# Performance work log

Measured on AMD Instinct MI355X. Metric: run time of the kernel, lower is better.

## Reference

```python
import jax, jax.numpy as jnp
import numpy as np

B, N, D, H = 8, 1024, 768, 12
HD = D // H
SCALE = HD ** -0.5

def setup_inputs() -> dict:
    key = jax.random.key(0)
    k1, k2, k3, k4 = jax.random.split(key, 4)
    x = jax.random.normal(k1, (B, N, D), dtype=jnp.float32)
    weight = jax.random.uniform(k2, (B, N), dtype=jnp.float32)
    W_qkv = jax.random.normal(k3, (D, 3 * D), dtype=jnp.float32) * (D ** -0.5)
    W_msa = jax.random.normal(k4, (D, D), dtype=jnp.float32) * (D ** -0.5)
    b_msa = jnp.zeros((D,), dtype=jnp.float32)
    return {"x": x, "weight": weight, "W_qkv": W_qkv, "W_msa": W_msa, "b_msa": b_msa}

def reference(x, weight, W_qkv, W_msa, b_msa):
    # QKV projection (no bias), then elementwise per-token gate
    qkv = jnp.einsum('bnd,de->bne', x, W_qkv)          # [B,N,3D]
    qkv = weight[:, :, None] * qkv
    qkv = qkv.reshape(B, N, 3, H, HD).transpose(2, 0, 3, 1, 4)  # [3,B,H,N,hd]
    q, k, v = qkv[0], qkv[1], qkv[2]
    A = jnp.einsum('bhnd,bhmd->bhnm', q, k) * SCALE    # [B,H,N,N]
    A = jax.nn.softmax(A, axis=-1)
    out = jnp.einsum('bhnm,bhmd->bhnd', A, v)          # [B,H,N,hd]
    out = out.transpose(0, 2, 1, 3).reshape(B, N, D)
    return jnp.einsum('bnd,de->bne', out, W_msa) + b_msa
```

## Files before the change

kernel.cpp:

```cpp
#include <hip/hip_runtime.h>
#include <hip/hip_bf16.h>


typedef __attribute__((ext_vector_type(8))) short bf8;
typedef __attribute__((ext_vector_type(4))) float f4;

#define QSCALE 0.1803368801111204f

static __device__ __forceinline__ short bf16_of(float f) {
    union { float f; unsigned u; } a; a.f = f;
    unsigned r = a.u + 0x7FFFu + ((a.u >> 16) & 1u);
    return (short)(r >> 16);
}

static __device__ __forceinline__ unsigned bfpk(float lo, float hi) {
    float2 t; t.x = lo; t.y = hi;
    __hip_bfloat162 b = __float22bfloat162_rn(t);
    union { __hip_bfloat162 b; unsigned u; } c; c.b = b;
    return c.u;
}

static __device__ __forceinline__ void async16(const short* g, short* l) {
    __builtin_amdgcn_global_load_lds(
        (const __attribute__((address_space(1))) void*)g,
        (__attribute__((address_space(3))) void*)l, 16, 0, 0);
}

__global__ __launch_bounds__(256) void k_cvt(const float* __restrict__ src,
                                             const float* __restrict__ gate,
                                             short* __restrict__ dst, int n8) {
    int i = blockIdx.x * 256 + threadIdx.x;
    if (i >= n8) return;
    const float g = gate[i / 96];
    const f4* sp = (const f4*)src;
    f4 a = sp[2 * i], b = sp[2 * i + 1];
    union { bf8 v; short h[8]; } o;
    o.h[0] = bf16_of(a[0] * g); o.h[1] = bf16_of(a[1] * g);
    o.h[2] = bf16_of(a[2] * g); o.h[3] = bf16_of(a[3] * g);
    o.h[4] = bf16_of(b[0] * g); o.h[5] = bf16_of(b[1] * g);
    o.h[6] = bf16_of(b[2] * g); o.h[7] = bf16_of(b[3] * g);
    ((bf8*)dst)[i] = o.v;
}

__global__ __launch_bounds__(256) void k_transpose(const float* __restrict__ w,
                                                   short* __restrict__ wt,
                                                   int K, int E) {
    __shared__ short t[64][65];
    const int k0 = blockIdx.y * 64, e0 = blockIdx.x * 64;
    const int tid = threadIdx.x;
#pragma unroll
    for (int p = 0; p < 16; ++p) {
        int idx = p * 256 + tid;
        int r = idx >> 6, c = idx & 63;
        t[r][c] = bf16_of(w[(k0 + r) * E + e0 + c]);
    }
    __syncthreads();
#pragma unroll
    for (int p = 0; p < 16; ++p) {
        int idx = p * 256 + tid;
        int r = idx >> 6, c = idx & 63;
        wt[(e0 + r) * K + k0 + c] = t[c][r];
    }
}

static __device__ __forceinline__ void gemm128(const short* __restrict__ gA,
                                               const short* __restrict__ gB,
                                               short* smem,
                                               f4 acc[4][4]) {
    const int tid = threadIdx.x, lane = tid & 63;
    const int l16 = lane & 15, quad = lane >> 4, rx = l16 & 7;
    const int wm = (tid >> 6) & 1, wn = tid >> 7;

    auto stage = [&](short* S, int k0) {
#pragma unroll
        for (int c = 0; c < 4; ++c) {
            int p = c * 256 + tid;
            int row = p >> 3, slot = p & 7;
            int gc = slot ^ (row & 7);
            async16(gA + row * 768 + k0 + gc * 8, S + p * 8);
            async16(gB + row * 768 + k0 + gc * 8, S + 8192 + p * 8);
        }
    };

    stage(smem, 0);
    for (int it = 0; it < 12; ++it) {
        __builtin_amdgcn_s_waitcnt(0);
        __syncthreads();
        short* Sc = smem + (it & 1) * 16384;
        if (it + 1 < 12) stage(smem + ((it + 1) & 1) * 16384, (it + 1) * 64);
        const short* As = Sc;
        const short* Bs = Sc + 8192;
#pragma unroll
        for (int ks = 0; ks < 2; ++ks) {
            bf8 af[4], bfr[4];
#pragma unroll
            for (int mt = 0; mt < 4; ++mt)
                af[mt] = *(const bf8*)(As + (wm * 64 + mt * 16 + l16) * 64 +
                                       (((ks * 4 + quad) ^ rx) * 8));
#pragma unroll
            for (int nt = 0; nt < 4; ++nt)
                bfr[nt] = *(const bf8*)(Bs + (wn * 64 + nt * 16 + l16) * 64 +
                                        (((ks * 4 + quad) ^ rx) * 8));
#pragma unroll
            for (int mt = 0; mt < 4; ++mt)
#pragma unroll
                for (int nt = 0; nt < 4; ++nt)
                    acc[mt][nt] = __builtin_amdgcn_mfma_f32_16x16x32_bf16(
                        af[mt], bfr[nt], acc[mt][nt], 0, 0, 0);
        }
    }
    __syncthreads();
}

__global__ __launch_bounds__(512, 2) void k_gemm_qkv(
        const short* __restrict__ xb, const short* __restrict__ wtq,
        short* __restrict__ qb, short* __restrict__ kb, short* __restrict__ vt) {
    __shared__ short lds[65536];
    const int tid = threadIdx.x, lane = tid & 63;
    const int l16 = lane & 15, quad = lane >> 4, rx = l16 & 7;
    const int wv = tid >> 6, wm = wv >> 2, wn = wv & 3;

    const int wg = blockIdx.x;
    const int swz = (wg & 7) * 36 + (wg >> 3);
    const int mI = swz / 9, nI = swz - mI * 9;
    const int m0 = mI * 256, n0 = nI * 256;

    const short* gA = xb + m0 * 768;
    const short* gB = wtq + n0 * 768;

    auto stageHalf = [&](int buf, int isB, int half, const short* gsrc, int k0) {
        short* dst = lds + buf * 32768 + isB * 16384 + half * 8192;
        const short* src = gsrc + half * 98304 + k0;
#pragma unroll
        for (int j = 0; j < 2; ++j) {
            int p = j * 512 + tid;
            int row = p >> 3;
            int gc = (p & 7) ^ (row & 7);
            async16(src + row * 768 + gc * 8, dst + p * 8);
        }
    };

    f4 z = {0.f, 0.f, 0.f, 0.f};
    f4 acc[8][4];
#pragma unroll
    for (int mt = 0; mt < 8; ++mt)
#pragma unroll
        for (int nt = 0; nt < 4; ++nt) acc[mt][nt] = z;

    stageHalf(0, 0, 0, gA, 0); stageHalf(0, 0, 1, gA, 0);
    stageHalf(0, 1, 0, gB, 0); stageHalf(0, 1, 1, gB, 0);
    stageHalf(1, 1, 0, gB, 64); stageHalf(1, 1, 1, gB, 64);
    asm volatile("s_waitcnt vmcnt(4)" ::: "memory");
    __builtin_amdgcn_s_barrier();

#pragma unroll 2
    for (int t = 0; t < 12; ++t) {
        const short* Ab = lds + (t & 1) * 32768;
        const short* Bb = Ab + 16384;
        bf8 af[4][2], bfr[4][2];

        auto rdA = [&](int mt, int ks) {
            return *(const bf8*)(Ab + (wm * 128 + mt * 16 + l16) * 64 +
                                 (((ks * 4 + quad) ^ rx) << 3));
        };
        auto rdB = [&](int nt, int ks) {
            return *(const bf8*)(Bb + (wn * 64 + nt * 16 + l16) * 64 +
                                 (((ks * 4 + quad) ^ rx) << 3));
        };

#pragma unroll
        for (int mt = 0; mt < 4; ++mt) { af[mt][0] = rdA(mt, 0); af[mt][1] = rdA(mt, 1); }
#pragma unroll
        for (int nt = 0; nt < 2; ++nt) { bfr[nt][0] = rdB(nt, 0); bfr[nt][1] = rdB(nt, 1); }
        if (t < 11) stageHalf((t + 1) & 1, 0, 0, gA, (t + 1) * 64);
        __builtin_amdgcn_s_barrier();
        __builtin_amdgcn_s_setprio(1);
#pragma unroll
        for (int mt = 0; mt < 4; ++mt)
#pragma unroll
            for (int nt = 0; nt < 2; ++nt) {
                acc[mt][nt] = __builtin_amdgcn_mfma_f32_16x16x32_bf16(
                    af[mt][0], bfr[nt][0], acc[mt][nt], 0, 0, 0);
                acc[mt][nt] = __builtin_amdgcn_mfma_f32_16x16x32_bf16(
                    af[mt][1], bfr[nt][1], acc[mt][nt], 0, 0, 0);
            }
        __builtin_amdgcn_s_setprio(0);
        __builtin_amdgcn_s_barrier();

#pragma unroll
        for (int nt = 2; nt < 4; ++nt) { bfr[nt][0] = rdB(nt, 0); bfr[nt][1] = rdB(nt, 1); }
        if (t < 11) stageHalf((t + 1) & 1, 0, 1, gA, (t + 1) * 64);
        __builtin_amdgcn_s_barrier();
        __builtin_amdgcn_s_setprio(1);
#pragma unroll
        for (int mt = 0; mt < 4; ++mt)
#pragma unroll
            for (int nt = 2; nt < 4; ++nt) {
                acc[mt][nt] = __builtin_amdgcn_mfma_f32_16x16x32_bf16(
                    af[mt][0], bfr[nt][0], acc[mt][nt], 0, 0, 0);
                acc[mt][nt] = __builtin_amdgcn_mfma_f32_16x16x32_bf16(
                    af[mt][1], bfr[nt][1], acc[mt][nt], 0, 0, 0);
            }
        __builtin_amdgcn_s_setprio(0);
        __builtin_amdgcn_s_barrier();

#pragma unroll
        for (int mt = 0; mt < 4; ++mt) { af[mt][0] = rdA(mt + 4, 0); af[mt][1] = rdA(mt + 4, 1); }
        if (t < 10) stageHalf(t & 1, 1, 0, gB, (t + 2) * 64);
        __builtin_amdgcn_s_barrier();
        __builtin_amdgcn_s_setprio(1);
#pragma unroll
        for (int mt = 0; mt < 4; ++mt)
#pragma unroll
            for (int nt = 2; nt < 4; ++nt) {
                acc[mt + 4][nt] = __builtin_amdgcn_mfma_f32_16x16x32_bf16(
                    af[mt][0], bfr[nt][0], acc[mt + 4][nt], 0, 0, 0);
                acc[mt + 4][nt] = __builtin_amdgcn_mfma_f32_16x16x32_bf16(
                    af[mt][1], bfr[nt][1], acc[mt + 4][nt], 0, 0, 0);
            }
        __builtin_amdgcn_s_setprio(0);
        __builtin_amdgcn_s_barrier();

        if (t < 10) stageHalf(t & 1, 1, 1, gB, (t + 2) * 64);
        __builtin_amdgcn_s_barrier();
        __builtin_amdgcn_s_setprio(1);
#pragma unroll
        for (int mt = 0; mt < 4; ++mt)
#pragma unroll
            for (int nt = 0; nt < 2; ++nt) {
                acc[mt + 4][nt] = __builtin_amdgcn_mfma_f32_16x16x32_bf16(
                    af[mt][0], bfr[nt][0], acc[mt + 4][nt], 0, 0, 0);
                acc[mt + 4][nt] = __builtin_amdgcn_mfma_f32_16x16x32_bf16(
                    af[mt][1], bfr[nt][1], acc[mt + 4][nt], 0, 0, 0);
            }
        __builtin_amdgcn_s_setprio(0);
        if (t < 10)       asm volatile("s_waitcnt vmcnt(4)" ::: "memory");
        else if (t == 10) asm volatile("s_waitcnt vmcnt(0)" ::: "memory");
        __builtin_amdgcn_s_barrier();
    }

    const int which = (n0 >= 1536) ? 2 : (n0 >= 768 ? 1 : 0);
    if (which < 2) {
#pragma unroll
        for (int mt = 0; mt < 8; ++mt) {
#pragma unroll
            for (int r = 0; r < 4; ++r) {
                const int row = m0 + wm * 128 + mt * 16 + quad * 4 + r;
                const int b = row >> 10, nn = row & 1023;
#pragma unroll
                for (int nt = 0; nt < 4; ++nt) {
                    const int ct = n0 + wn * 64 + nt * 16;
                    const int h = (ct - which * 768) >> 6;
                    const int hh = b * 12 + h;
                    const int hd = (ct & 63) + l16;
                    const float val = acc[mt][nt][r];
                    if (which == 0)
                        qb[(hh * 1024 + nn) * 64 + hd] = bf16_of(val * QSCALE);
                    else
                        kb[(hh * 1024 + nn) * 64 + hd] = bf16_of(val);
                }
            }
        }
    } else {
        const int b = m0 >> 10, nn0 = m0 & 1023;
        const int dg0 = n0 - 1536;
#pragma unroll
        for (int ch = 0; ch < 2; ++ch) {
            if ((wn >> 1) == ch) {
#pragma unroll
                for (int mt = 0; mt < 8; ++mt)
#pragma unroll
                    for (int nt = 0; nt < 4; ++nt)
#pragma unroll
                        for (int r = 0; r < 4; ++r) {
                            const int rl = wm * 128 + mt * 16 + quad * 4 + r;
                            const int cl = wn * 64 + nt * 16 + l16 - ch * 128;
                            lds[cl * 264 + rl] = bf16_of(acc[mt][nt][r]);
                        }
            }
            __syncthreads();
#pragma unroll
            for (int ph = 0; ph < 8; ++ph) {
                const int idx = ph * 512 + tid;
                const int cl = idx >> 5, ck = idx & 31;
                const int dg = dg0 + ch * 128 + cl;
                const int h = dg >> 6, hd = dg & 63;
                bf8 valv = *(const bf8*)(lds + cl * 264 + ck * 8);
                *(bf8*)(vt + ((b * 12 + h) * 64 + hd) * 1024 + nn0 + ck * 8) = valv;
            }
            __syncthreads();
        }
    }
}

__global__ __launch_bounds__(256) void k_gemm_final(
        const short* __restrict__ attn, const short* __restrict__ wtm,
        const float* __restrict__ bias, float* __restrict__ out) {
    __shared__ short smem[32768];
    const int lane = threadIdx.x & 63;
    const int l16 = lane & 15, quad = lane >> 4;
    const int wm = (threadIdx.x >> 6) & 1, wn = threadIdx.x >> 7;
    const int m0 = blockIdx.y * 128, n0 = blockIdx.x * 128;
    f4 z = {0.f, 0.f, 0.f, 0.f};
    f4 acc[4][4] = {{z,z,z,z},{z,z,z,z},{z,z,z,z},{z,z,z,z}};
    gemm128(attn + m0 * 768, wtm + n0 * 768, smem, acc);
#pragma unroll
    for (int mt = 0; mt < 4; ++mt) {
#pragma unroll
        for (int r = 0; r < 4; ++r) {
            const int row = m0 + wm * 64 + mt * 16 + quad * 4 + r;
#pragma unroll
            for (int nt = 0; nt < 4; ++nt) {
                const int e = n0 + wn * 64 + nt * 16 + l16;
                out[row * 768 + e] = acc[mt][nt][r] + bias[e];
            }
        }
    }
}

__global__ __launch_bounds__(512) void k_attn(const short* __restrict__ qb,
                                              const short* __restrict__ kb,
                                              const short* __restrict__ vt,
                                              short* __restrict__ attn) {
    __shared__ short Ks[2][4096];
    __shared__ short Vs[2][4096];
    const int tid = threadIdx.x, wave = tid >> 6, lane = tid & 63;
    const int l16 = lane & 15, quad = lane >> 4;
    const int bh = blockIdx.x;
    const int b = bh / 12, h = bh - b * 12;
    const int m_base = blockIdx.y * 128 + wave * 16;
    const short* qh = qb + bh * 65536;
    const short* kh = kb + bh * 65536;
    const short* vh = vt + bh * 65536;

    const int rA = ((l16 >> 2) << 3) + (l16 & 3);
    const int fK = (((rA >> 3) & 1) << 2) + (rA & 3);
    const int sK = (quad ^ fK) * 8;
    const int oAlo = rA * 64 + sK;
    const int oAhi = rA * 64 + (sK ^ 32);
    const int oBlo = oAlo + 256, oBhi = oAhi + 256;
    const int fV = (((l16 >> 3) & 1) << 2) + (l16 & 3);
    const int oV = l16 * 64 + ((quad ^ fV) * 8);

    const short* qp = qh + (m_base + l16) * 64 + quad * 8;
    bf8 qf0 = *(const bf8*)(qp);
    bf8 qf1 = *(const bf8*)(qp + 32);

    union { bf8 v; short h[8]; } onef;
#pragma unroll
    for (int i = 0; i < 8; ++i) onef.h[i] = (short)0x3F80;

    f4 z = {0.f, 0.f, 0.f, 0.f};
    f4 acc[4] = {z, z, z, z};
    f4 accl = z;

    auto stage = [&](int buf, int j0) {
        int idx = tid;
        int row = idx >> 3;
        int fr = (((row >> 3) & 1) << 2) + (row & 3);
        int gc = (idx & 7) ^ fr;
        async16(kh + (j0 + row) * 64 + gc * 8, Ks[buf] + idx * 8);
        async16(vh + row * 1024 + j0 + gc * 8, Vs[buf] + idx * 8);
    };

    stage(0, 0);
    int cur = 0;
    for (int it = 0; it < 16; ++it) {
        __builtin_amdgcn_s_waitcnt(0);
        __syncthreads();
        if (it + 1 < 16) stage(cur ^ 1, (it + 1) * 64);
        const short* Kc = Ks[cur];
        const short* Vc = Vs[cur];

#pragma unroll
        for (int jj = 0; jj < 64; jj += 32) {
            const short* kjj = Kc + jj * 64;
            bf8 kAlo = *(const bf8*)(kjj + oAlo);
            bf8 kAhi = *(const bf8*)(kjj + oAhi);
            bf8 kBlo = *(const bf8*)(kjj + oBlo);
            bf8 kBhi = *(const bf8*)(kjj + oBhi);

            f4 sA = z, sB = z;
            sA = __builtin_amdgcn_mfma_f32_16x16x32_bf16(kAlo, qf0, sA, 0, 0, 0);
            sA = __builtin_amdgcn_mfma_f32_16x16x32_bf16(kAhi, qf1, sA, 0, 0, 0);
            sB = __builtin_amdgcn_mfma_f32_16x16x32_bf16(kBlo, qf0, sB, 0, 0, 0);
            sB = __builtin_amdgcn_mfma_f32_16x16x32_bf16(kBhi, qf1, sB, 0, 0, 0);
            float a0 = __builtin_amdgcn_exp2f(sA[0]);
            float a1 = __builtin_amdgcn_exp2f(sA[1]);
            float a2 = __builtin_amdgcn_exp2f(sA[2]);
            float a3 = __builtin_amdgcn_exp2f(sA[3]);
            float b0 = __builtin_amdgcn_exp2f(sB[0]);
            float b1 = __builtin_amdgcn_exp2f(sB[1]);
            float b2 = __builtin_amdgcn_exp2f(sB[2]);
            float b3 = __builtin_amdgcn_exp2f(sB[3]);
            union { bf8 v; unsigned u[4]; } p;
            p.u[0] = bfpk(a0, a1); p.u[1] = bfpk(a2, a3);
            p.u[2] = bfpk(b0, b1); p.u[3] = bfpk(b2, b3);
            accl = __builtin_amdgcn_mfma_f32_16x16x32_bf16(
                onef.v, p.v, accl, 0, 0, 0);

#pragma unroll
            for (int dt = 0; dt < 4; ++dt) {
                bf8 vf = *(const bf8*)(Vc + dt * 1024 + (oV ^ (jj ? 32 : 0)));
                acc[dt] = __builtin_amdgcn_mfma_f32_16x16x32_bf16(
                    vf, p.v, acc[dt], 0, 0, 0);
            }
        }
        cur ^= 1;
    }

    const float inv = 1.f / accl[0];
    const int row = (b << 10) + m_base + l16;
    short* op = attn + row * 768 + h * 64 + quad * 4;
#pragma unroll
    for (int dt = 0; dt < 4; ++dt)
#pragma unroll
        for (int r = 0; r < 4; ++r)
            op[dt * 16 + r] = bf16_of(acc[dt][r] * inv);
}

extern "C" void kernel_launch(void* const* d_in, const int* in_sizes, int n_in,
                              void* d_out, int out_size, void* d_ws, size_t ws_size,
                              hipStream_t stream) {
    const float* x    = (const float*)d_in[0];
    const float* gate = (const float*)d_in[1];
    const float* Wqkv = (const float*)d_in[2];
    const float* Wmsa = (const float*)d_in[3];
    const float* bmsa = (const float*)d_in[4];
    float* out = (float*)d_out;

    char* ws = (char*)d_ws;
    short* xb  = (short*)(ws);
    short* wtq = (short*)(ws + 12582912);
    short* wtm = (short*)(ws + 16121856);
    short* qb  = (short*)(ws + 17301504);
    short* kb  = (short*)(ws + 29884416);
    short* vt  = (short*)(ws + 42467328);
    short* attn = xb;

    k_cvt<<<3072, 256, 0, stream>>>(x, gate, xb, 786432);
    k_transpose<<<dim3(36, 12), 256, 0, stream>>>(Wqkv, wtq, 768, 2304);
    k_transpose<<<dim3(12, 12), 256, 0, stream>>>(Wmsa, wtm, 768, 768);
    k_gemm_qkv<<<288, 512, 0, stream>>>(xb, wtq, qb, kb, vt);
    k_attn<<<dim3(96, 8), 512, 0, stream>>>(qb, kb, vt, attn);
    k_gemm_final<<<dim3(6, 64), 256, 0, stream>>>(attn, wtm, bmsa, out);
}
```

Before: 196.4 us.

## Retile QKV GEMM to 256x288 tiles so grid matches 256 CUs

The QKV projection GEMM changes from 256x256 tiles on a 288-block grid to 256x288 tiles on a 256-block grid. This matches the block count to the MI355X's CU count and avoids a partial second wave. The warp layout becomes 4x2 with each wave computing 64x144 (4x9 MFMA fragments), and staging and waitcnt counts are adjusted for the extra B rows. The epilogue is rewritten so tiles spanning the Q/K/V boundaries are handled per fragment, with V transposed through LDS in 96-column passes. The costs are more LDS (up to 139KB per block), more accumulator registers, and tiles that straddle output segments.

```diff
diff --git a/kernel.cpp b/kernel.cpp
--- a/kernel.cpp
+++ b/kernel.cpp
@@ -115,22 +115,22 @@
 __global__ __launch_bounds__(512, 2) void k_gemm_qkv(
         const short* __restrict__ xb, const short* __restrict__ wtq,
         short* __restrict__ qb, short* __restrict__ kb, short* __restrict__ vt) {
-    __shared__ short lds[65536];
+    __shared__ short lds[69632];
     const int tid = threadIdx.x, lane = tid & 63;
     const int l16 = lane & 15, quad = lane >> 4, rx = l16 & 7;
-    const int wv = tid >> 6, wm = wv >> 2, wn = wv & 3;
+    const int wv = tid >> 6, wm = wv >> 1, wn = wv & 1;
 
     const int wg = blockIdx.x;
-    const int swz = (wg & 7) * 36 + (wg >> 3);
-    const int mI = swz / 9, nI = swz - mI * 9;
-    const int m0 = mI * 256, n0 = nI * 256;
+    const int swz = (wg & 7) * 32 + (wg >> 3);
+    const int mI = swz >> 3, nI = swz & 7;
+    const int m0 = mI * 256, n0 = nI * 288;
 
     const short* gA = xb + m0 * 768;
     const short* gB = wtq + n0 * 768;
 
-    auto stageHalf = [&](int buf, int isB, int half, const short* gsrc, int k0) {
-        short* dst = lds + buf * 32768 + isB * 16384 + half * 8192;
-        const short* src = gsrc + half * 98304 + k0;
+    auto stageA = [&](int buf, int half, int k0) {
+        short* dst = lds + buf * 34816 + half * 8192;
+        const short* src = gA + half * 98304 + k0;
 #pragma unroll
         for (int j = 0; j < 2; ++j) {
             int p = j * 512 + tid;
@@ -139,156 +139,175 @@
             async16(src + row * 768 + gc * 8, dst + p * 8);
         }
     };
+    auto stageB = [&](int buf, int half, int k0) {
+        short* dst = lds + buf * 34816 + 16384 + half * 9216;
+        const short* src = gB + half * 110592 + k0;
+#pragma unroll
+        for (int j = 0; j < 2; ++j) {
+            int p = j * 512 + tid;
+            int row = p >> 3;
+            int gc = (p & 7) ^ (row & 7);
+            async16(src + row * 768 + gc * 8, dst + p * 8);
+        }
+        if (tid < 128) {
+            int p = 1024 + tid;
+            int row = p >> 3;
+            int gc = (p & 7) ^ (row & 7);
+            async16(src + row * 768 + gc * 8, dst + p * 8);
+        }
+    };
 
     f4 z = {0.f, 0.f, 0.f, 0.f};
-    f4 acc[8][4];
-#pragma unroll
-    for (int mt = 0; mt < 8; ++mt)
-#pragma unroll
-        for (int nt = 0; nt < 4; ++nt) acc[mt][nt] = z;
-
-    stageHalf(0, 0, 0, gA, 0); stageHalf(0, 0, 1, gA, 0);
-    stageHalf(0, 1, 0, gB, 0); stageHalf(0, 1, 1, gB, 0);
-    stageHalf(1, 1, 0, gB, 64); stageHalf(1, 1, 1, gB, 64);
-    asm volatile("s_waitcnt vmcnt(4)" ::: "memory");
+    f4 acc[4][9];
+#pragma unroll
+    for (int mf = 0; mf < 4; ++mf)
+#pragma unroll
+        for (int nf = 0; nf < 9; ++nf) acc[mf][nf] = z;
+
+    stageA(0, 0, 0); stageA(0, 1, 0);
+    stageB(0, 0, 0); stageB(0, 1, 0);
+    stageB(1, 0, 64);
+    if (wv < 2) asm volatile("s_waitcnt vmcnt(3)" ::: "memory");
+    else        asm volatile("s_waitcnt vmcnt(2)" ::: "memory");
     __builtin_amdgcn_s_barrier();
 
 #pragma unroll 2
     for (int t = 0; t < 12; ++t) {
-        const short* Ab = lds + (t & 1) * 32768;
+        const short* Ab = lds + (t & 1) * 34816;
         const short* Bb = Ab + 16384;
-        bf8 af[4][2], bfr[4][2];
-
-        auto rdA = [&](int mt, int ks) {
-            return *(const bf8*)(Ab + (wm * 128 + mt * 16 + l16) * 64 +
+        auto rdA = [&](int mf, int ks) {
+            return *(const bf8*)(Ab + (wm * 64 + mf * 16 + l16) * 64 +
                                  (((ks * 4 + quad) ^ rx) << 3));
         };
-        auto rdB = [&](int nt, int ks) {
-            return *(const bf8*)(Bb + (wn * 64 + nt * 16 + l16) * 64 +
+        auto rdB = [&](int nf, int ks) {
+            return *(const bf8*)(Bb + (wn * 144 + nf * 16 + l16) * 64 +
                                  (((ks * 4 + quad) ^ rx) << 3));
         };
-
-#pragma unroll
-        for (int mt = 0; mt < 4; ++mt) { af[mt][0] = rdA(mt, 0); af[mt][1] = rdA(mt, 1); }
-#pragma unroll
-        for (int nt = 0; nt < 2; ++nt) { bfr[nt][0] = rdB(nt, 0); bfr[nt][1] = rdB(nt, 1); }
-        if (t < 11) stageHalf((t + 1) & 1, 0, 0, gA, (t + 1) * 64);
+        bf8 af[4][2], bfr[9][2];
+
+#pragma unroll
+        for (int mf = 0; mf < 2; ++mf) { af[mf][0] = rdA(mf, 0); af[mf][1] = rdA(mf, 1); }
+#pragma unroll
+        for (int nf = 0; nf < 5; ++nf) { bfr[nf][0] = rdB(nf, 0); bfr[nf][1] = rdB(nf, 1); }
+        if (t < 11) stageB((t + 1) & 1, 1, (t + 1) * 64);
         __builtin_amdgcn_s_barrier();
         __builtin_amdgcn_s_setprio(1);
 #pragma unroll
-        for (int mt = 0; mt < 4; ++mt)
-#pragma unroll
-            for (int nt = 0; nt < 2; ++nt) {
-                acc[mt][nt] = __builtin_amdgcn_mfma_f32_16x16x32_bf16(
-                    af[mt][0], bfr[nt][0], acc[mt][nt], 0, 0, 0);
-                acc[mt][nt] = __builtin_amdgcn_mfma_f32_16x16x32_bf16(
-                    af[mt][1], bfr[nt][1], acc[mt][nt], 0, 0, 0);
+        for (int mf = 0; mf < 2; ++mf)
+#pragma unroll
+            for (int nf = 0; nf < 5; ++nf) {
+                acc[mf][nf] = __builtin_amdgcn_mfma_f32_16x16x32_bf16(
+                    af[mf][0], bfr[nf][0], acc[mf][nf], 0, 0, 0);
+                acc[mf][nf] = __builtin_amdgcn_mfma_f32_16x16x32_bf16(
+                    af[mf][1], bfr[nf][1], acc[mf][nf], 0, 0, 0);
             }
         __builtin_amdgcn_s_setprio(0);
         __builtin_amdgcn_s_barrier();
 
 #pragma unroll
-        for (int nt = 2; nt < 4; ++nt) { bfr[nt][0] = rdB(nt, 0); bfr[nt][1] = rdB(nt, 1); }
-        if (t < 11) stageHalf((t + 1) & 1, 0, 1, gA, (t + 1) * 64);
+        for (int mf = 2; mf < 4; ++mf) { af[mf][0] = rdA(mf, 0); af[mf][1] = rdA(mf, 1); }
+        if (t < 11) stageA((t + 1) & 1, 0, (t + 1) * 64);
         __builtin_amdgcn_s_barrier();
         __builtin_amdgcn_s_setprio(1);
 #pragma unroll
-        for (int mt = 0; mt < 4; ++mt)
-#pragma unroll
-            for (int nt = 2; nt < 4; ++nt) {
-                acc[mt][nt] = __builtin_amdgcn_mfma_f32_16x16x32_bf16(
-                    af[mt][0], bfr[nt][0], acc[mt][nt], 0, 0, 0);
-                acc[mt][nt] = __builtin_amdgcn_mfma_f32_16x16x32_bf16(
-                    af[mt][1], bfr[nt][1], acc[mt][nt], 0, 0, 0);
+        for (int mf = 2; mf < 4; ++mf)
+#pragma unroll
+            for (int nf = 0; nf < 5; ++nf) {
+                acc[mf][nf] = __builtin_amdgcn_mfma_f32_16x16x32_bf16(
+                    af[mf][0], bfr[nf][0], acc[mf][nf], 0, 0, 0);
+                acc[mf][nf] = __builtin_amdgcn_mfma_f32_16x16x32_bf16(
+                    af[mf][1], bfr[nf][1], acc[mf][nf], 0, 0, 0);
             }
         __builtin_amdgcn_s_setprio(0);
         __builtin_amdgcn_s_barrier();
 
 #pragma unroll
-        for (int mt = 0; mt < 4; ++mt) { af[mt][0] = rdA(mt + 4, 0); af[mt][1] = rdA(mt + 4, 1); }
-        if (t < 10) stageHalf(t & 1, 1, 0, gB, (t + 2) * 64);
+        for (int nf = 5; nf < 9; ++nf) { bfr[nf][0] = rdB(nf, 0); bfr[nf][1] = rdB(nf, 1); }
+        if (t < 11) stageA((t + 1) & 1, 1, (t + 1) * 64);
         __builtin_amdgcn_s_barrier();
         __builtin_amdgcn_s_setprio(1);
 #pragma unroll
-        for (int mt = 0; mt < 4; ++mt)
-#pragma unroll
-            for (int nt = 2; nt < 4; ++nt) {
-                acc[mt + 4][nt] = __builtin_amdgcn_mfma_f32_16x16x32_bf16(
-                    af[mt][0], bfr[nt][0], acc[mt + 4][nt], 0, 0, 0);
-                acc[mt + 4][nt] = __builtin_amdgcn_mfma_f32_16x16x32_bf16(
-                    af[mt][1], bfr[nt][1], acc[mt + 4][nt], 0, 0, 0);
+        for (int mf = 0; mf < 2; ++mf)
+#pragma unroll
+            for (int nf = 5; nf < 9; ++nf) {
+                acc[mf][nf] = __builtin_amdgcn_mfma_f32_16x16x32_bf16(
+                    af[mf][0], bfr[nf][0], acc[mf][nf], 0, 0, 0);
+                acc[mf][nf] = __builtin_amdgcn_mfma_f32_16x16x32_bf16(
+                    af[mf][1], bfr[nf][1], acc[mf][nf], 0, 0, 0);
             }
         __builtin_amdgcn_s_setprio(0);
         __builtin_amdgcn_s_barrier();
 
-        if (t < 10) stageHalf(t & 1, 1, 1, gB, (t + 2) * 64);
+        if (t < 10) stageB(t & 1, 0, (t + 2) * 64);
         __builtin_amdgcn_s_barrier();
         __builtin_amdgcn_s_setprio(1);
 #pragma unroll
-        for (int mt = 0; mt < 4; ++mt)
-#pragma unroll
-            for (int nt = 0; nt < 2; ++nt) {
-                acc[mt + 4][nt] = __builtin_amdgcn_mfma_f32_16x16x32_bf16(
-                    af[mt][0], bfr[nt][0], acc[mt + 4][nt], 0, 0, 0);
-                acc[mt + 4][nt] = __builtin_amdgcn_mfma_f32_16x16x32_bf16(
-                    af[mt][1], bfr[nt][1], acc[mt + 4][nt], 0, 0, 0);
+        for (int mf = 2; mf < 4; ++mf)
+#pragma unroll
+            for (int nf = 5; nf < 9; ++nf) {
+                acc[mf][nf] = __builtin_amdgcn_mfma_f32_16x16x32_bf16(
+                    af[mf][0], bfr[nf][0], acc[mf][nf], 0, 0, 0);
+                acc[mf][nf] = __builtin_amdgcn_mfma_f32_16x16x32_bf16(
+                    af[mf][1], bfr[nf][1], acc[mf][nf], 0, 0, 0);
             }
         __builtin_amdgcn_s_setprio(0);
-        if (t < 10)       asm volatile("s_waitcnt vmcnt(4)" ::: "memory");
-        else if (t == 10) asm volatile("s_waitcnt vmcnt(0)" ::: "memory");
-        __builtin_amdgcn_s_barrier();
-    }
-
-    const int which = (n0 >= 1536) ? 2 : (n0 >= 768 ? 1 : 0);
-    if (which < 2) {
-#pragma unroll
-        for (int mt = 0; mt < 8; ++mt) {
-#pragma unroll
-            for (int r = 0; r < 4; ++r) {
-                const int row = m0 + wm * 128 + mt * 16 + quad * 4 + r;
-                const int b = row >> 10, nn = row & 1023;
-#pragma unroll
-                for (int nt = 0; nt < 4; ++nt) {
-                    const int ct = n0 + wn * 64 + nt * 16;
-                    const int h = (ct - which * 768) >> 6;
-                    const int hh = b * 12 + h;
-                    const int hd = (ct & 63) + l16;
-                    const float val = acc[mt][nt][r];
-                    if (which == 0)
-                        qb[(hh * 1024 + nn) * 64 + hd] = bf16_of(val * QSCALE);
-                    else
-                        kb[(hh * 1024 + nn) * 64 + hd] = bf16_of(val);
+        if (t < 10) {
+            if (wv < 2) asm volatile("s_waitcnt vmcnt(3)" ::: "memory");
+            else        asm volatile("s_waitcnt vmcnt(2)" ::: "memory");
+        } else if (t == 10) {
+            asm volatile("s_waitcnt vmcnt(0)" ::: "memory");
+        }
+        __builtin_amdgcn_s_barrier();
+    }
+
+    const int bI = m0 >> 10, nn0 = m0 & 1023;
+#pragma unroll
+    for (int nf = 0; nf < 9; ++nf) {
+        const int ct = n0 + wn * 144 + nf * 16;
+        if (ct < 1536) {
+            const int which = (ct >= 768) ? 1 : 0;
+            const int h = (ct - which * 768) >> 6;
+            const int hd = (ct & 63) + l16;
+            short* dst = (which ? kb : qb) + ((bI * 12 + h) * 1024) * 64 + hd;
+#pragma unroll
+            for (int mf = 0; mf < 4; ++mf)
+#pragma unroll
+                for (int r = 0; r < 4; ++r) {
+                    const int nn = nn0 + wm * 64 + mf * 16 + quad * 4 + r;
+                    const float val = acc[mf][nf][r];
+                    dst[nn * 64] = bf16_of(which ? val : val * QSCALE);
                 }
-            }
-        }
-    } else {
-        const int b = m0 >> 10, nn0 = m0 & 1023;
-        const int dg0 = n0 - 1536;
-#pragma unroll
-        for (int ch = 0; ch < 2; ++ch) {
-            if ((wn >> 1) == ch) {
-#pragma unroll
-                for (int mt = 0; mt < 8; ++mt)
-#pragma unroll
-                    for (int nt = 0; nt < 4; ++nt)
-#pragma unroll
-                        for (int r = 0; r < 4; ++r) {
-                            const int rl = wm * 128 + mt * 16 + quad * 4 + r;
-                            const int cl = wn * 64 + nt * 16 + l16 - ch * 128;
-                            lds[cl * 264 + rl] = bf16_of(acc[mt][nt][r]);
-                        }
-            }
-            __syncthreads();
-#pragma unroll
-            for (int ph = 0; ph < 8; ++ph) {
-                const int idx = ph * 512 + tid;
-                const int cl = idx >> 5, ck = idx & 31;
-                const int dg = dg0 + ch * 128 + cl;
-                const int h = dg >> 6, hd = dg & 63;
-                bf8 valv = *(const bf8*)(lds + cl * 264 + ck * 8);
-                *(bf8*)(vt + ((b * 12 + h) * 64 + hd) * 1024 + nn0 + ck * 8) = valv;
-            }
-            __syncthreads();
+        }
+    }
+    const int vstart = (n0 >= 1536) ? n0 : 1536;
+    const int npass = (n0 + 288 > vstart) ? (n0 + 288 - vstart) / 96 : 0;
+    for (int p = 0; p < npass; ++p) {
+        __syncthreads();
+        const int c0 = vstart + p * 96;
+#pragma unroll
+        for (int nf = 0; nf < 9; ++nf) {
+            const int ct = n0 + wn * 144 + nf * 16;
+            if (ct >= c0 && ct < c0 + 96) {
+                const int lc = ct - c0 + l16;
+#pragma unroll
+                for (int mf = 0; mf < 4; ++mf)
+#pragma unroll
+                    for (int r = 0; r < 4; ++r) {
+                        const int rl = wm * 64 + mf * 16 + quad * 4 + r;
+                        lds[lc * 264 + rl] = bf16_of(acc[mf][nf][r]);
+                    }
+            }
+        }
+        __syncthreads();
+        const int vg0 = c0 - 1536;
+#pragma unroll
+        for (int u = 0; u < 6; ++u) {
+            const int idx = u * 512 + tid;
+            const int lc = idx >> 5, ck = idx & 31;
+            const int vg = vg0 + lc;
+            const int h = vg >> 6, hd = vg & 63;
+            bf8 vv = *(const bf8*)(lds + lc * 264 + ck * 8);
+            *(bf8*)(vt + ((bI * 12 + h) * 64 + hd) * 1024 + nn0 + ck * 8) = vv;
         }
     }
 }
@@ -441,7 +460,7 @@
     k_cvt<<<3072, 256, 0, stream>>>(x, gate, xb, 786432);
     k_transpose<<<dim3(36, 12), 256, 0, stream>>>(Wqkv, wtq, 768, 2304);
     k_transpose<<<dim3(12, 12), 256, 0, stream>>>(Wmsa, wtm, 768, 768);
-    k_gemm_qkv<<<288, 512, 0, stream>>>(xb, wtq, qb, kb, vt);
+    k_gemm_qkv<<<256, 512, 0, stream>>>(xb, wtq, qb, kb, vt);
     k_attn<<<dim3(96, 8), 512, 0, stream>>>(qb, kb, vt, attn);
     k_gemm_final<<<dim3(6, 64), 256, 0, stream>>>(attn, wtm, bmsa, out);
 }
```

Measured after the change: 186.1 us. 5.3% less time.
